# Kernel optimization log

Measured on AMD Instinct MI355X. Metric: run time of the kernel, lower is better.

Reference implementation:

```python
import jax, jax.numpy as jnp
import numpy as np

N = 48
K = 16
COLS = N - K  # 32
B = 65536
FEAT = K * COLS + COLS * COLS + K * K + min(K, COLS)  # 1808


def setup_inputs() -> dict:
    key = jax.random.key(0)
    ks = jax.random.split(key, 9)
    def lin(kw, fan_in, fan_out):
        bound = 1.0 / np.sqrt(fan_in)
        return jax.random.uniform(kw, (fan_in, fan_out), jnp.float32, -bound, bound)
    x = jax.random.normal(ks[0], (B, K * COLS), dtype=jnp.float32)
    W1 = lin(ks[1], FEAT, 256); b1 = jnp.zeros((256,), jnp.float32)
    W2 = lin(ks[2], 256, 128);  b2 = jnp.zeros((128,), jnp.float32)
    W3 = lin(ks[3], 128, 64);   b3 = jnp.zeros((64,), jnp.float32)
    W4 = lin(ks[4], 64, 1);     b4 = jnp.zeros((1,), jnp.float32)
    return {"x": x, "W1": W1, "b1": b1, "W2": W2, "b2": b2,
            "W3": W3, "b3": b3, "W4": W4, "b4": b4}


def reference(x, W1, b1, W2, b2, W3, b3, W4, b4):
    Bn = x.shape[0]
    P = x.reshape(Bn, K, COLS)                      # [B,k,cols]
    gram_cols = jnp.einsum('bki,bkj->bij', P, P)    # P^T P, [B,cols,cols]
    gram_rows = jnp.einsum('bik,bjk->bij', P, P)    # P P^T, [B,k,k]
    svd_vals = jnp.linalg.svd(P, compute_uv=False)  # [B,min(k,cols)]
    feats = jnp.concatenate([
        x,
        gram_cols.reshape(Bn, -1),
        gram_rows.reshape(Bn, -1),
        svd_vals,
    ], axis=1)                                       # [B,1808]
    h = jax.nn.relu(feats @ W1 + b1)
    h = jax.nn.relu(h @ W2 + b2)
    h = jax.nn.relu(h @ W3 + b3)
    return h @ W4 + b4                               # [B,1]
```

## Files before the change

kernel.cpp:

```cpp
#include <hip/hip_runtime.h>
#include <hip/hip_bf16.h>
#include <cstdint>
#include <cstddef>

typedef unsigned short u16;
typedef unsigned int u32;
typedef short short8 __attribute__((ext_vector_type(8)));
typedef short short4v __attribute__((ext_vector_type(4)));
typedef __bf16 bf16x8 __attribute__((ext_vector_type(8)));
typedef float v4f __attribute__((ext_vector_type(4)));
typedef float v16f __attribute__((ext_vector_type(16)));

#define NSAMP 65536
#define FEAT_PAD 1824


__device__ __forceinline__ u16 f2bf(float f) {
  union { float f; u32 u; } v; v.f = f;
  u32 r = (v.u + 0x7FFFu + ((v.u >> 16) & 1u)) >> 16;
  return (u16)r;
}
__device__ __forceinline__ u16 f2bf_h(float f) {
  return __builtin_bit_cast(u16, (__bf16)f);
}
__device__ __forceinline__ float bf2f(u16 h) {
  union { u32 u; float f; } v; v.u = ((u32)h) << 16;
  return v.f;
}

__device__ __forceinline__ v4f mfma16(short8 a, short8 b, v4f c) {
  return __builtin_amdgcn_mfma_f32_16x16x32_bf16(
      __builtin_bit_cast(bf16x8, a), __builtin_bit_cast(bf16x8, b), c, 0, 0, 0);
}
__device__ __forceinline__ v16f mfma32(short8 a, short8 b, v16f c) {
  return __builtin_amdgcn_mfma_f32_32x32x16_bf16(
      __builtin_bit_cast(bf16x8, a), __builtin_bit_cast(bf16x8, b), c, 0, 0, 0);
}

typedef __attribute__((address_space(1))) const void* gas_ptr;
typedef __attribute__((address_space(3))) void* las_ptr;
__device__ __forceinline__ void gl_lds16(const void* g, void* l) {
  __builtin_amdgcn_global_load_lds((gas_ptr)g, (las_ptr)l, 16, 0, 0);
}

__global__ void prep_kernel(const float* __restrict__ W1, const float* __restrict__ W2,
                            const float* __restrict__ W3,
                            u16* __restrict__ w1t, u16* __restrict__ w2t, u16* __restrict__ w3t) {
  int idx = blockIdx.x * 256 + threadIdx.x;
  if (idx < 256 * FEAT_PAD) {
    int n = idx / FEAT_PAD, kp = idx % FEAT_PAD;
    int k;
    if (kp < 512) {
      k = kp;
    } else if (kp < 1536) {
      int t = kp - 512, ln = t >> 4, rr = t & 15;
      int jj = ln & 31, q2 = ln >> 5;
      int i = (rr & 3) + 8 * (rr >> 2) + 4 * q2;
      k = 512 + i * 32 + jj;
    } else if (kp < 1792) {
      int t = kp - 1536, ln = t >> 2, rr = t & 3;
      int jj = ln & 15;
      int i = (ln >> 4) * 4 + rr;
      k = 1536 + i * 16 + jj;
    } else {
      k = kp;
    }
    size_t addr = (size_t)(n >> 4) * 29184 + (kp >> 3) * 128 + (n & 15) * 8 + (kp & 7);
    w1t[addr] = (kp < 1808) ? f2bf(W1[(size_t)k * 256 + n]) : (u16)0;
  }
  if (idx < 128 * 256) {
    int n = idx / 256, k = idx % 256;
    size_t addr = (size_t)(n >> 4) * 4096 + (k >> 3) * 128 + (n & 15) * 8 + (k & 7);
    w2t[addr] = f2bf(W2[k * 128 + n]);
  }
  if (idx < 64 * 128) {
    int n = idx / 128, k = idx % 128;
    size_t addr = (size_t)(n >> 4) * 2048 + (k >> 3) * 128 + (n & 15) * 8 + (k & 7);
    w3t[addr] = f2bf(W3[k * 64 + n]);
  }
}

__device__ __forceinline__ void svd4(const v4f* aR, u16* tb, int s0, int lane) {
  const int j = lane & 15, bse = lane & 48, q = lane >> 4;
  const int jr = (j - 4 * q) & 15;
  int sig[16];
#pragma unroll
  for (int m = 0; m < 16; ++m) sig[m] = bse + ((m + 4 * q) & 15);

  float a[16];
#pragma unroll
  for (int c = 0; c < 4; ++c) {
    const int srcq = (q - c) & 3;
    const int rd = ((q + c) & 3) * 16 + j;
#pragma unroll
    for (int r = 0; r < 4; ++r) {
      float lo = (srcq & 1) ? aR[1][r] : aR[0][r];
      float hi = (srcq & 1) ? aR[3][r] : aR[2][r];
      float sel = (srcq & 2) ? hi : lo;
      a[c * 4 + r] = __shfl(sel, rd);
    }
  }

  float es[16];
#pragma unroll
  for (int i = 0; i < 16; ++i) es[i] = 0.f;

#pragma unroll
  for (int step = 0; step < 14; ++step) {
    const int i = 15 - step, l = i - 1;
    float xm = (jr <= l) ? a[i] : 0.f;
    float xa[16];
#pragma unroll
    for (int m = 0; m < 16; ++m) xa[m] = (m < i) ? __shfl(xm, sig[m]) : 0.f;
    float ha = 0.f, hb = 0.f;
#pragma unroll
    for (int m = 0; m < 16; m += 2) if (m < i) ha = fmaf(xa[m], xa[m], ha);
#pragma unroll
    for (int m = 1; m < 16; m += 2) if (m < i) hb = fmaf(xa[m], xa[m], hb);
    float h = ha + hb;
    float ul = xa[l];
    float sq = __builtin_amdgcn_sqrtf(h);
    float alpha = (ul >= 0.f) ? -sq : sq;
    float denom = h - ul * alpha;
    float beta = (h > 1e-30f) ? __builtin_amdgcn_rcpf(denom) : 0.f;
    float vq = (jr < l) ? xm : ((jr == l) ? (xm - alpha) : 0.f);
    xa[l] -= alpha;
    es[i] = alpha;
    float pa = 0.f, pb = 0.f;
#pragma unroll
    for (int m = 0; m < 16; m += 2) if (m < i) pa = fmaf(a[m], xa[m], pa);
#pragma unroll
    for (int m = 1; m < 16; m += 2) if (m < i) pb = fmaf(a[m], xa[m], pb);
    float p = (pa + pb) * beta;
    float pp[16];
#pragma unroll
    for (int m = 0; m < 16; ++m) pp[m] = (m < i) ? __shfl(p, sig[m]) : 0.f;
    float Ka = 0.f, Kb = 0.f;
#pragma unroll
    for (int m = 0; m < 16; m += 2) if (m < i) Ka = fmaf(pp[m], xa[m], Ka);
#pragma unroll
    for (int m = 1; m < 16; m += 2) if (m < i) Kb = fmaf(pp[m], xa[m], Kb);
    float Ks = (Ka + Kb) * (0.5f * beta);
    float wsc = p - Ks * vq;
#pragma unroll
    for (int m = 0; m < 16; ++m) {
      if (m < i) {
        float wm = pp[m] - Ks * xa[m];
        a[m] -= xa[m] * wsc + wm * vq;
      }
    }
  }
  es[1] = __shfl(a[1], sig[0]);

  float dd[16];
#pragma unroll
  for (int m = 0; m < 16; ++m) dd[m] = __shfl(a[m], sig[m]);
  float e2a[16];
  e2a[0] = 0.f;
#pragma unroll
  for (int k = 1; k < 16; ++k) e2a[k] = es[k] * es[k] + 1e-30f;
  float dmax = dd[0], emax = 0.f;
#pragma unroll
  for (int m = 1; m < 16; ++m) dmax = fmaxf(dmax, dd[m]);
#pragma unroll
  for (int k = 1; k < 16; ++k) emax = fmaxf(emax, fabsf(es[k]));

  const float scl = 0.03125f;
#pragma unroll
  for (int m = 0; m < 16; ++m) dd[m] *= scl;
#pragma unroll
  for (int k = 1; k < 16; ++k) e2a[k] *= (scl * scl);

  float lo = 0.f, hi = (dmax + 2.f * emax + 1e-6f) * scl;
#pragma unroll 1
  for (int iter = 0; iter < 13; ++iter) {
    float mid = 0.5f * (lo + hi);
    float pm1 = 1.f, pc = dd[0] - mid;
    u32 cnt = __builtin_bit_cast(u32, pc) >> 31;
#pragma unroll
    for (int k = 1; k < 16; ++k) {
      float t = e2a[k] * pm1;
      float pn = fmaf(dd[k] - mid, pc, -t);
      cnt += ((__builtin_bit_cast(u32, pn) ^ __builtin_bit_cast(u32, pc)) >> 31);
      pm1 = pc; pc = pn;
    }
    if ((int)cnt > jr) hi = mid; else lo = mid;
  }
  float lam = 0.5f * (lo + hi) * 32.f;
  int t = 15 - jr;
  int s = s0 + q;
  tb[(size_t)(224 + (t >> 3)) * 128 + (s & 15) * 8 + (t & 7)] =
      f2bf_h(__builtin_amdgcn_sqrtf(fmaxf(lam, 0.f)));
}

__global__ __launch_bounds__(256) void feat_kernel(const float* __restrict__ x,
                                                   u16* __restrict__ feats) {
  const int lane = threadIdx.x & 63;
  const int wv = threadIdx.x >> 6;
  const int wid = blockIdx.x;
  const int l15 = lane & 15, l31 = lane & 31, q4 = lane >> 4, q2 = lane >> 5;
  const int pbase = l15 * 32 + q4 * 8;
  u16* tb = feats + (size_t)wid * 29184;

  short8 sx[4], sc0[4], sc1[4];
  short4v sr4[4];
  v4f aR[4];
#pragma unroll
  for (int r8 = 0; r8 < 4; ++r8) {
    const int s = wid * 16 + wv * 4 + r8;
    const float* xs = x + (size_t)s * 512;
    float4 p0 = *(const float4*)(xs + pbase);
    float4 p1 = *(const float4*)(xs + pbase + 4);
    float t[8];
#pragma unroll
    for (int j = 0; j < 8; ++j) t[j] = xs[(q2 * 8 + j) * 32 + l31];

    short8 fp, ft;
    fp[0] = (short)f2bf_h(p0.x); fp[1] = (short)f2bf_h(p0.y);
    fp[2] = (short)f2bf_h(p0.z); fp[3] = (short)f2bf_h(p0.w);
    fp[4] = (short)f2bf_h(p1.x); fp[5] = (short)f2bf_h(p1.y);
    fp[6] = (short)f2bf_h(p1.z); fp[7] = (short)f2bf_h(p1.w);
#pragma unroll
    for (int j = 0; j < 8; ++j) ft[j] = (short)f2bf_h(t[j]);

    v4f accR; v16f accC;
#pragma unroll
    for (int r = 0; r < 4; ++r) accR[r] = 0.f;
#pragma unroll
    for (int r = 0; r < 16; ++r) accC[r] = 0.f;
    accR = mfma16(fp, fp, accR);
    accC = mfma32(ft, ft, accC);

    sx[r8] = fp;
#pragma unroll
    for (int r = 0; r < 8; ++r) { sc0[r8][r] = (short)f2bf_h(accC[r]); sc1[r8][r] = (short)f2bf_h(accC[r + 8]); }
#pragma unroll
    for (int r = 0; r < 4; ++r) sr4[r8][r] = (short)f2bf_h(accR[r]);
    aR[r8] = accR;
  }

  const int ho = wv * 4;
#pragma unroll
  for (int r8 = 0; r8 < 4; ++r8)
    *(short8*)(tb + (l15 * 4 + q4) * 128 + (ho + r8) * 8) = sx[r8];
#pragma unroll
  for (int r8 = 0; r8 < 4; ++r8)
    *(short8*)(tb + (64 + lane * 2) * 128 + (ho + r8) * 8) = sc0[r8];
#pragma unroll
  for (int r8 = 0; r8 < 4; ++r8)
    *(short8*)(tb + (65 + lane * 2) * 128 + (ho + r8) * 8) = sc1[r8];
#pragma unroll
  for (int r8 = 0; r8 < 4; ++r8)
    *(short4v*)(tb + (192 + (lane >> 1)) * 128 + (lane & 1) * 4 + (ho + r8) * 8) = sr4[r8];

  if (wv == 3 && lane < 32) {
    short8 z;
#pragma unroll
    for (int j = 0; j < 8; ++j) z[j] = 0;
    *(short8*)(tb + 226 * 128 + lane * 8) = z;
  }

  svd4(aR, tb, wid * 16 + ho, lane);
}

__global__ __launch_bounds__(256, 2) void gemm1_kernel(const u16* __restrict__ feats,
                                                       const u16* __restrict__ w1t,
                                                       const float* __restrict__ b1,
                                                       u16* __restrict__ h1) {
  __shared__ __align__(16) u16 At[2 * 8 * 512];
  __shared__ __align__(16) u16 Bt[2 * 16 * 512];
  const int tid = threadIdx.x, lane = tid & 63, wv = tid >> 6;
  const int l15 = lane & 15, q4 = lane >> 4;
  const int m0 = blockIdx.x * 128;
  const int wm = (wv & 1) * 64, wn = (wv >> 1) * 128;

  const u16* gA[2];
#pragma unroll
  for (int j = 0; j < 2; ++j)
    gA[j] = feats + (size_t)((m0 >> 4) + wv * 2 + j) * 29184 + lane * 8;
  const u16* gB[4];
#pragma unroll
  for (int j = 0; j < 4; ++j)
    gB[j] = w1t + (size_t)(wv * 4 + j) * 29184 + lane * 8;

  v4f acc[4][8];
#pragma unroll
  for (int mt = 0; mt < 4; ++mt)
#pragma unroll
    for (int nt = 0; nt < 8; ++nt)
#pragma unroll
      for (int r = 0; r < 4; ++r) acc[mt][nt][r] = 0.f;

  const int NT = FEAT_PAD / 32;

  {
#pragma unroll
    for (int j = 0; j < 2; ++j) gl_lds16(gA[j], At + (wv * 2 + j) * 512);
#pragma unroll
    for (int j = 0; j < 4; ++j) gl_lds16(gB[j], Bt + (wv * 4 + j) * 512);
  }
  __syncthreads();

  int cur = 0;
  for (int t = 0; t < NT; ++t) {
    if (t + 1 < NT) {
      const int go = (t + 1) * 512;
      const int nb = cur ^ 1;
#pragma unroll
      for (int j = 0; j < 2; ++j) gl_lds16(gA[j] + go, At + nb * 4096 + (wv * 2 + j) * 512);
#pragma unroll
      for (int j = 0; j < 4; ++j) gl_lds16(gB[j] + go, Bt + nb * 8192 + (wv * 4 + j) * 512);
    }

    const u16* Ab = At + cur * 4096;
    const u16* Bb = Bt + cur * 8192;
    short8 af[4], bfr[8];
#pragma unroll
    for (int mt = 0; mt < 4; ++mt)
      af[mt] = *(const short8*)(Ab + ((wv & 1) * 4 + mt) * 512 + q4 * 128 + l15 * 8);
#pragma unroll
    for (int nt = 0; nt < 8; ++nt)
      bfr[nt] = *(const short8*)(Bb + ((wv >> 1) * 8 + nt) * 512 + q4 * 128 + l15 * 8);
#pragma unroll
    for (int mt = 0; mt < 4; ++mt)
#pragma unroll
      for (int nt = 0; nt < 8; ++nt)
        acc[mt][nt] = mfma16(af[mt], bfr[nt], acc[mt][nt]);

    __syncthreads();
    cur ^= 1;
  }

#pragma unroll
  for (int mt = 0; mt < 4; ++mt)
#pragma unroll
    for (int nt = 0; nt < 8; ++nt) {
      int col = wn + nt * 16 + l15;
      float bias = b1[col];
#pragma unroll
      for (int r = 0; r < 4; ++r) {
        int row = m0 + wm + mt * 16 + q4 * 4 + r;
        h1[(size_t)row * 256 + col] = f2bf_h(fmaxf(acc[mt][nt][r] + bias, 0.f));
      }
    }
}

__global__ __launch_bounds__(256, 2) void gemm23_kernel(
    const u16* __restrict__ h1, const u16* __restrict__ w2t, const float* __restrict__ b2,
    const u16* __restrict__ w3t, const float* __restrict__ b3,
    const float* __restrict__ w4, const float* __restrict__ b4, float* __restrict__ out) {
  __shared__ __align__(16) u16 H2[128 * 136];
  const int tid = threadIdx.x, lane = tid & 63, wv = tid >> 6;
  const int l15 = lane & 15, q4 = lane >> 4;
  const int m0 = blockIdx.x * 128;

  const u16* pA[2];
#pragma unroll
  for (int mt = 0; mt < 2; ++mt)
    pA[mt] = h1 + (size_t)(m0 + wv * 32 + mt * 16 + l15) * 256 + q4 * 8;
  const u16* pB[8];
#pragma unroll
  for (int nt = 0; nt < 8; ++nt)
    pB[nt] = w2t + (size_t)nt * 4096 + q4 * 128 + l15 * 8;

  v4f acc[2][8];
#pragma unroll
  for (int mt = 0; mt < 2; ++mt)
#pragma unroll
    for (int nt = 0; nt < 8; ++nt)
#pragma unroll
      for (int r = 0; r < 4; ++r) acc[mt][nt][r] = 0.f;

#pragma unroll
  for (int kk = 0; kk < 8; ++kk) {
    short8 af[2], bfr[8];
#pragma unroll
    for (int mt = 0; mt < 2; ++mt) af[mt] = *(const short8*)(pA[mt] + kk * 32);
#pragma unroll
    for (int nt = 0; nt < 8; ++nt) bfr[nt] = *(const short8*)(pB[nt] + kk * 512);
#pragma unroll
    for (int mt = 0; mt < 2; ++mt)
#pragma unroll
      for (int nt = 0; nt < 8; ++nt)
        acc[mt][nt] = mfma16(af[mt], bfr[nt], acc[mt][nt]);
  }

#pragma unroll
  for (int mt = 0; mt < 2; ++mt)
#pragma unroll
    for (int nt = 0; nt < 8; ++nt) {
      int c = nt * 16 + l15;
      float bias = b2[c];
#pragma unroll
      for (int r = 0; r < 4; ++r) {
        int rl = wv * 32 + mt * 16 + q4 * 4 + r;
        H2[rl * 136 + c] = f2bf_h(fmaxf(acc[mt][nt][r] + bias, 0.f));
      }
    }

  v4f acc2[2][4];
#pragma unroll
  for (int mt = 0; mt < 2; ++mt)
#pragma unroll
    for (int nt = 0; nt < 4; ++nt)
#pragma unroll
      for (int r = 0; r < 4; ++r) acc2[mt][nt][r] = 0.f;
#pragma unroll
  for (int kk = 0; kk < 4; ++kk) {
    short8 af2[2], bf2v[4];
#pragma unroll
    for (int mt = 0; mt < 2; ++mt)
      af2[mt] = *(const short8*)(H2 + (wv * 32 + mt * 16 + l15) * 136 + kk * 32 + q4 * 8);
#pragma unroll
    for (int nt = 0; nt < 4; ++nt)
      bf2v[nt] = *(const short8*)(w3t + (size_t)nt * 2048 + (kk * 4 + q4) * 128 + l15 * 8);
#pragma unroll
    for (int mt = 0; mt < 2; ++mt)
#pragma unroll
      for (int nt = 0; nt < 4; ++nt)
        acc2[mt][nt] = mfma16(af2[mt], bf2v[nt], acc2[mt][nt]);
  }

  float b4v = b4[0];
#pragma unroll
  for (int mt = 0; mt < 2; ++mt)
#pragma unroll
    for (int r = 0; r < 4; ++r) {
      float p = 0.f;
#pragma unroll
      for (int nt = 0; nt < 4; ++nt) {
        int c = nt * 16 + l15;
        float h3 = fmaxf(acc2[mt][nt][r] + b3[c], 0.f);
        p += h3 * w4[c];
      }
      p += __shfl_xor(p, 1);
      p += __shfl_xor(p, 2);
      p += __shfl_xor(p, 4);
      p += __shfl_xor(p, 8);
      if (l15 == 0) {
        int row = m0 + wv * 32 + mt * 16 + q4 * 4 + r;
        out[row] = p + b4v;
      }
    }
}

extern "C" void kernel_launch(void* const* d_in, const int* in_sizes, int n_in,
                              void* d_out, int out_size, void* d_ws, size_t ws_size,
                              hipStream_t stream) {
  const float* x  = (const float*)d_in[0];
  const float* W1 = (const float*)d_in[1];
  const float* b1 = (const float*)d_in[2];
  const float* W2 = (const float*)d_in[3];
  const float* b2 = (const float*)d_in[4];
  const float* W3 = (const float*)d_in[5];
  const float* b3 = (const float*)d_in[6];
  const float* W4 = (const float*)d_in[7];
  const float* b4 = (const float*)d_in[8];
  float* out = (float*)d_out;

  char* ws = (char*)d_ws;
  u16* feats = (u16*)ws;
  u16* h1    = (u16*)(ws + 239075328ull);
  u16* w1t   = (u16*)(ws + 239075328ull + 33554432ull);
  u16* w2t   = (u16*)(ws + 239075328ull + 33554432ull + 933888ull);
  u16* w3t   = (u16*)(ws + 239075328ull + 33554432ull + 933888ull + 65536ull);

  prep_kernel<<<1824, 256, 0, stream>>>(W1, W2, W3, w1t, w2t, w3t);
  feat_kernel<<<4096, 256, 0, stream>>>(x, feats);
  gemm1_kernel<<<512, 256, 0, stream>>>(feats, w1t, b1, h1);
  gemm23_kernel<<<512, 256, 0, stream>>>(h1, w2t, b2, w3t, b3, W4, b4, out);
}
```

Baseline: 418.2 us.

## Keep two K-tiles in flight in GEMM1 with partial vmcnt waits

The layer-1 GEMM main loop now issues global-to-LDS loads for tiles 0 and 1 up front. Each iteration waits with s_waitcnt vmcnt(6), so only the current tile has to land, then synchronises with raw s_barrier calls. The next-but-one tile is loaded into the buffer just consumed, after a second barrier. The aim is to stop __syncthreads from draining every outstanding memory op each iteration, so load latency overlaps compute more fully. The cost is hand-coded waitcnt counts that depend on exactly six loads per stage, which is fragile if the load count or compiler scheduling changes.

```diff
diff --git a/kernel.cpp b/kernel.cpp
--- a/kernel.cpp
+++ b/kernel.cpp
@@ -293,43 +293,55 @@
 
   const int NT = FEAT_PAD / 32;
 
-  {
-#pragma unroll
-    for (int j = 0; j < 2; ++j) gl_lds16(gA[j], At + (wv * 2 + j) * 512);
-#pragma unroll
-    for (int j = 0; j < 4; ++j) gl_lds16(gB[j], Bt + (wv * 4 + j) * 512);
-  }
-  __syncthreads();
+#define STAGE1(t, buf)                                                          \
+  {                                                                             \
+    const int _go = (t) * 512;                                                  \
+    _Pragma("unroll")                                                           \
+    for (int j = 0; j < 2; ++j)                                                 \
+      gl_lds16(gA[j] + _go, At + (buf) * 4096 + (wv * 2 + j) * 512);            \
+    _Pragma("unroll")                                                           \
+    for (int j = 0; j < 4; ++j)                                                 \
+      gl_lds16(gB[j] + _go, Bt + (buf) * 8192 + (wv * 4 + j) * 512);            \
+  }
+
+#define COMPUTE1(buf)                                                           \
+  {                                                                             \
+    const u16* Ab = At + (buf) * 4096;                                          \
+    const u16* Bb = Bt + (buf) * 8192;                                          \
+    short8 af[4], bfr[8];                                                       \
+    _Pragma("unroll")                                                           \
+    for (int mt = 0; mt < 4; ++mt)                                              \
+      af[mt] = *(const short8*)(Ab + ((wv & 1) * 4 + mt) * 512 + q4 * 128 + l15 * 8); \
+    _Pragma("unroll")                                                           \
+    for (int nt = 0; nt < 8; ++nt)                                              \
+      bfr[nt] = *(const short8*)(Bb + ((wv >> 1) * 8 + nt) * 512 + q4 * 128 + l15 * 8); \
+    _Pragma("unroll")                                                           \
+    for (int mt = 0; mt < 4; ++mt)                                              \
+      _Pragma("unroll")                                                         \
+      for (int nt = 0; nt < 8; ++nt)                                            \
+        acc[mt][nt] = mfma16(af[mt], bfr[nt], acc[mt][nt]);                     \
+  }
+
+  STAGE1(0, 0);
+  STAGE1(1, 1);
 
   int cur = 0;
-  for (int t = 0; t < NT; ++t) {
-    if (t + 1 < NT) {
-      const int go = (t + 1) * 512;
-      const int nb = cur ^ 1;
-#pragma unroll
-      for (int j = 0; j < 2; ++j) gl_lds16(gA[j] + go, At + nb * 4096 + (wv * 2 + j) * 512);
-#pragma unroll
-      for (int j = 0; j < 4; ++j) gl_lds16(gB[j] + go, Bt + nb * 8192 + (wv * 4 + j) * 512);
-    }
-
-    const u16* Ab = At + cur * 4096;
-    const u16* Bb = Bt + cur * 8192;
-    short8 af[4], bfr[8];
-#pragma unroll
-    for (int mt = 0; mt < 4; ++mt)
-      af[mt] = *(const short8*)(Ab + ((wv & 1) * 4 + mt) * 512 + q4 * 128 + l15 * 8);
-#pragma unroll
-    for (int nt = 0; nt < 8; ++nt)
-      bfr[nt] = *(const short8*)(Bb + ((wv >> 1) * 8 + nt) * 512 + q4 * 128 + l15 * 8);
-#pragma unroll
-    for (int mt = 0; mt < 4; ++mt)
-#pragma unroll
-      for (int nt = 0; nt < 8; ++nt)
-        acc[mt][nt] = mfma16(af[mt], bfr[nt], acc[mt][nt]);
-
-    __syncthreads();
+#pragma unroll 1
+  for (int t = 0; t < NT - 1; ++t) {
+    asm volatile("s_waitcnt vmcnt(6)" ::: "memory");
+    __builtin_amdgcn_sched_barrier(0);
+    __builtin_amdgcn_s_barrier();
+    COMPUTE1(cur);
+    __builtin_amdgcn_s_barrier();
+    if (t + 2 < NT) STAGE1(t + 2, cur);
     cur ^= 1;
   }
+  asm volatile("s_waitcnt vmcnt(0)" ::: "memory");
+  __builtin_amdgcn_sched_barrier(0);
+  __builtin_amdgcn_s_barrier();
+  COMPUTE1(cur);
+#undef STAGE1
+#undef COMPUTE1
 
 #pragma unroll
   for (int mt = 0; mt < 4; ++mt)
```

Result: faster. 408.3 us (-2.4%).
